# Kernel tuning notes

Hardware: AMD Instinct MI355X
Metric: run time of the kernel (lower is better)

The kernel has to match this reference:

```python
import jax, jax.numpy as jnp
import numpy as np

B, M, IN, H, D = 64, 512, 256, 4, 64
N = B * M
E = N * 16


def setup_inputs() -> dict:
    key = jax.random.key(0)
    ks = jax.random.split(key, 12)
    s = 1.0 / np.sqrt(IN)
    return {
        "query_input": jax.random.normal(ks[0], (N, IN), jnp.float32),
        "source_input": jax.random.normal(ks[1], (N, IN), jnp.float32),
        "edge_weight": jax.random.uniform(ks[2], (E,), jnp.float32),
        "Wq_w": jax.random.normal(ks[3], (IN, H * D), jnp.float32) * s,
        "Wq_b": jax.random.normal(ks[4], (H * D,), jnp.float32) * s,
        "Wk_w": jax.random.normal(ks[5], (IN, H * D), jnp.float32) * s,
        "Wk_b": jax.random.normal(ks[6], (H * D,), jnp.float32) * s,
        "Wv_w": jax.random.normal(ks[7], (IN, H * D), jnp.float32) * s,
        "Wv_b": jax.random.normal(ks[8], (H * D,), jnp.float32) * s,
        "n_nodes": jnp.full((B,), M, jnp.int32),
        "edge_index": jax.random.randint(ks[9], (2, E), 0, N, jnp.int32),
    }


def reference(query_input, source_input, edge_weight, Wq_w, Wq_b, Wk_w, Wk_b, Wv_w, Wv_b, n_nodes, edge_index):
    # projections -> [N, H, D]
    q = (query_input @ Wq_w + Wq_b).reshape(N, H, D)
    k = (source_input @ Wk_w + Wk_b).reshape(N, H, D)
    v = (source_input @ Wv_w + Wv_b).reshape(N, H, D)

    # 'simple' kernel attention. Global L2 normalization (torch.norm over whole tensor).
    qn = q / jnp.linalg.norm(q)
    kn = k / jnp.linalg.norm(k)
    # equal-size graphs: padding + mask reduces exactly to a reshape [B, M, H, D]
    q_pad = qn.reshape(B, M, H, D)
    k_pad = kn.reshape(B, M, H, D)
    v_pad = v.reshape(B, M, H, D)
    kv = jnp.einsum('bmhk,bmhv->bhkv', k_pad, v_pad)          # per-graph K^T V
    v_sum = v_pad.sum(axis=1)                                  # [B, H, D] scatter_add over batch
    k_sum = k_pad.sum(axis=1)                                  # [B, H, D]
    numer = jnp.einsum('bmhk,bhkv->bmhv', q_pad, kv) + v_sum[:, None]
    denom = jnp.einsum('bmhk,bhk->bmh', q_pad, k_sum) + n_nodes.astype(q.dtype)[:, None, None]
    attn = (numer / denom[..., None]).reshape(N, H, D)

    # gcn_conv on value: out[c] = sum_{e: col_e = c} w_e * rsqrt(deg[col_e]*deg[row_e]) * v[row_e]
    row, col = edge_index[0], edge_index[1]
    deg = jax.ops.segment_sum(jnp.ones((E,), jnp.float32), col, num_segments=N)
    val = edge_weight / jnp.sqrt(deg[col] * deg[row])
    val = jnp.nan_to_num(val, nan=0.0, posinf=0.0, neginf=0.0)
    gcn = jax.ops.segment_sum(val[:, None, None] * v[row], col, num_segments=N)

    return (attn + gcn).mean(axis=1)  # mean over heads -> [N, D]
```

## Files before the change

### kernel.cpp

```cpp
#include <hip/hip_runtime.h>
#include <hip/hip_bf16.h>

#define NN 32768
#define BB 64
#define MM 512
#define HH 4
#define DD 64
#define INF 256
#define HD 256
#define EE 524288
#define XSZ 8388608

typedef unsigned short ushort;
typedef unsigned int uint;
typedef short s16x8 __attribute__((ext_vector_type(8)));
typedef ushort u16x8 __attribute__((ext_vector_type(8)));
typedef float f32x4 __attribute__((ext_vector_type(4)));

__device__ __forceinline__ ushort f2bf(float f) {
    uint u = __float_as_uint(f);
    return (ushort)((u + 0x7fffu + ((u >> 16) & 1u)) >> 16);
}
__device__ __forceinline__ float bf2f(ushort u) {
    return __uint_as_float((uint)u << 16);
}
__device__ __forceinline__ uint pkbf(float x, float y) {
    __hip_bfloat162 h = __float22bfloat162_rn(make_float2(x, y));
    return *(uint*)&h;
}

#define GLD16(gp, lp) __builtin_amdgcn_global_load_lds( \
    (const __attribute__((address_space(1))) void*)(gp), \
    (__attribute__((address_space(3))) void*)(lp), 16, 0, 0)

__global__ __launch_bounds__(256) void prep_kernel(
    const float* __restrict__ Wq, const float* __restrict__ Wk,
    const float* __restrict__ Wv, ushort* __restrict__ WT,
    const int* __restrict__ ei, int* __restrict__ deg,
    const float* __restrict__ Xq, const float* __restrict__ Xs,
    ushort* __restrict__ xq16, ushort* __restrict__ xs16)
{
    const int bid = blockIdx.x;
    if (bid < 768) {
        const int id = bid * 256 + threadIdx.x;
        const int mat = id >> 16, rem = id & 65535;
        const int n = rem >> 8, kk = rem & 255;
        const float* W = (mat == 0) ? Wq : (mat == 1) ? Wk : Wv;
        WT[id] = f2bf(W[kk * 256 + n]);
    } else if (bid < 2816) {
        const int e = (bid - 768) * 256 + threadIdx.x;
        atomicAdd(&deg[ei[EE + e]], 1);
    } else {
        const size_t id = (size_t)(bid - 2816) * 256 + threadIdx.x;
        const size_t o8 = id * 8;
        const float* src; ushort* dst; size_t o;
        if (o8 < XSZ) { src = Xq; dst = xq16; o = o8; }
        else          { src = Xs; dst = xs16; o = o8 - XSZ; }
        const float4 f0 = *(const float4*)(src + o);
        const float4 f1 = *(const float4*)(src + o + 4);
        u16x8 r;
        r[0] = f2bf(f0.x); r[1] = f2bf(f0.y); r[2] = f2bf(f0.z); r[3] = f2bf(f0.w);
        r[4] = f2bf(f1.x); r[5] = f2bf(f1.y); r[6] = f2bf(f1.z); r[7] = f2bf(f1.w);
        *(u16x8*)(dst + o) = r;
    }
}

__global__ __launch_bounds__(256) void qkv_scan(
    const ushort* __restrict__ Xq16, const ushort* __restrict__ Xs16,
    const ushort* __restrict__ WT,
    const float* __restrict__ bq, const float* __restrict__ bk,
    const float* __restrict__ bv,
    ushort* __restrict__ qo, ushort* __restrict__ ko, ushort* __restrict__ vo,
    float* __restrict__ sumsq,
    const int* __restrict__ deg, int* __restrict__ offsets)
{
    __shared__ ushort As[3][128 * 32];
    __shared__ ushort Bs[3][128 * 32];
    __shared__ float wred[4];
    __shared__ int part[256];

    const int id = blockIdx.x;
    const int t = threadIdx.x;

    if (id == 1536) {
        const int base = t * 128;
        int s = 0;
        for (int i = 0; i < 128; ++i) s += deg[base + i];
        part[t] = s;
        __syncthreads();
        for (int off = 1; off < 256; off <<= 1) {
            int a = part[t];
            int b2 = (t >= off) ? part[t - off] : 0;
            __syncthreads();
            part[t] = a + b2;
            __syncthreads();
        }
        int run = (t == 0) ? 0 : part[t - 1];
        for (int i = 0; i < 128; ++i) { offsets[base + i] = run; run += deg[base + i]; }
        if (t == 255) offsets[NN] = run;
        return;
    }

    const int vv = (id & 7) * 192 + (id >> 3);
    const int rt = vv / 6, ct = vv % 6;
    const int wsel = ct >> 1;
    const ushort* A16 = (wsel == 0) ? Xq16 : Xs16;
    const ushort* W   = WT + (size_t)wsel * 65536;
    const float* bias = (wsel == 0) ? bq : (wsel == 1) ? bk : bv;
    ushort* C         = (wsel == 0) ? qo : (wsel == 1) ? ko : vo;
    const int row0 = rt * 128;
    const int col0 = (ct & 1) * 128;

    const int l = t & 63, w = t >> 6;
    const int fr = l & 15, q4 = l >> 4;
    const int wr = (w & 1) * 64, wc = (w >> 1) * 64;

    const int srow = (w << 4) + (l >> 2);
    const int scol = (l & 3) << 3;
    const ushort* ga = &A16[(size_t)(row0 + srow) * INF + scol];
    const ushort* gb = &W  [(size_t)(col0 + srow) * INF + scol];
    const int lbase = (w << 9);

    f32x4 acc[4][4] = {};

#define QKV_STAGE(bufi, k0) \
    GLD16(ga + (k0),            &As[bufi][lbase]); \
    GLD16(ga + (k0) + 64 * INF, &As[bufi][2048 + lbase]); \
    GLD16(gb + (k0),            &Bs[bufi][lbase]); \
    GLD16(gb + (k0) + 64 * INF, &Bs[bufi][2048 + lbase]);

#define QKV_COMPUTE(bufi) { \
    const int kg = q4 * 8; \
    s16x8 af[4], bfr[4]; \
    _Pragma("unroll") \
    for (int i = 0; i < 4; ++i) \
        af[i] = *(const s16x8*)&As[bufi][(wr + i * 16 + fr) * 32 + kg]; \
    _Pragma("unroll") \
    for (int j = 0; j < 4; ++j) \
        bfr[j] = *(const s16x8*)&Bs[bufi][(wc + j * 16 + fr) * 32 + kg]; \
    _Pragma("unroll") \
    for (int i = 0; i < 4; ++i) \
    _Pragma("unroll") \
        for (int j = 0; j < 4; ++j) \
            acc[i][j] = __builtin_amdgcn_mfma_f32_16x16x32_bf16( \
                af[i], bfr[j], acc[i][j], 0, 0, 0); }

#define WAIT4 asm volatile("s_waitcnt vmcnt(4)" ::: "memory")
#define WAIT0 asm volatile("s_waitcnt vmcnt(0)" ::: "memory")
#define BAR   __builtin_amdgcn_s_barrier()

    QKV_STAGE(0, 0)
    QKV_STAGE(1, 32)

    WAIT4; BAR; QKV_STAGE(2,  64) QKV_COMPUTE(0)
    WAIT4; BAR; QKV_STAGE(0,  96) QKV_COMPUTE(1)
    WAIT4; BAR; QKV_STAGE(1, 128) QKV_COMPUTE(2)
    WAIT4; BAR; QKV_STAGE(2, 160) QKV_COMPUTE(0)
    WAIT4; BAR; QKV_STAGE(0, 192) QKV_COMPUTE(1)
    WAIT4; BAR; QKV_STAGE(1, 224) QKV_COMPUTE(2)
    WAIT4; BAR;                   QKV_COMPUTE(0)
    WAIT0; BAR;                   QKV_COMPUTE(1)

    float loc = 0.f;
#pragma unroll
    for (int j = 0; j < 4; ++j) {
        const int colg = col0 + wc + j * 16 + fr;
        const float bj = bias[colg];
#pragma unroll
        for (int i = 0; i < 4; ++i) {
            const int rowg = row0 + wr + i * 16 + q4 * 4;
#pragma unroll
            for (int m = 0; m < 4; ++m) {
                float cv = acc[i][j][m] + bj;
                loc += cv * cv;
                C[(size_t)(rowg + m) * HD + colg] = f2bf(cv);
            }
        }
    }
    if (wsel < 2) {
#pragma unroll
        for (int off = 32; off > 0; off >>= 1) loc += __shfl_down(loc, off, 64);
        if (l == 0) wred[w] = loc;
        __syncthreads();
        if (t == 0) atomicAdd(&sumsq[wsel], wred[0] + wred[1] + wred[2] + wred[3]);
    }
}

#define KVP 72
__global__ __launch_bounds__(256) void kv_vbar_bucket(
    const ushort* __restrict__ k16, const ushort* __restrict__ v16,
    ushort* __restrict__ kv16, float* __restrict__ ksum_f, float* __restrict__ vsum_f,
    float* __restrict__ vbar,
    const int* __restrict__ ei, const float* __restrict__ ew,
    const int* __restrict__ deg, const int* __restrict__ offsets,
    int* __restrict__ cursor, int2* __restrict__ pairbuf)
{
    __shared__ ushort kT[64 * KVP];
    __shared__ ushort vT[64 * KVP];
    const int bid = blockIdx.x;
    const int t = threadIdx.x;

    if (bid >= 1280) {
        const int e = (bid - 1280) * 256 + t;
        const int row = ei[e], col = ei[EE + e];
        const long long prod = (long long)deg[row] * (long long)deg[col];
        float val = 0.f;
        if (prod > 0) val = ew[e] * __frsqrt_rn((float)prod);
        const int pos = atomicAdd(&cursor[col], 1);
        pairbuf[offsets[col] + pos] = make_int2(row, __float_as_int(val));
        return;
    }
    if (bid >= 256) {
        const int idx = (bid - 256) * 256 + t;
        const int n = idx >> 3, d0 = (idx & 7) * 8;
        const ushort* vr = &v16[(size_t)n * HD + d0];
        u16x8 v0 = *(const u16x8*)(vr);
        u16x8 v1 = *(const u16x8*)(vr + 64);
        u16x8 v2 = *(const u16x8*)(vr + 128);
        u16x8 v3 = *(const u16x8*)(vr + 192);
        float o[8];
#pragma unroll
        for (int j = 0; j < 8; ++j)
            o[j] = 0.25f * (bf2f(v0[j]) + bf2f(v1[j]) + bf2f(v2[j]) + bf2f(v3[j]));
        float* vb = &vbar[(size_t)n * DD + d0];
        *(float4*)(vb)     = make_float4(o[0], o[1], o[2], o[3]);
        *(float4*)(vb + 4) = make_float4(o[4], o[5], o[6], o[7]);
        return;
    }

    const int h = bid & 3, b = bid >> 2;
    const int l = t & 63, w = t >> 6;
    const size_t base = (size_t)b * MM * HD + (size_t)h * DD;

    const int fr = l & 15, q4 = l >> 4, kg = q4 * 8;
    const int wr2 = (w & 1) * 32, wc2 = (w >> 1) * 32;
    s16x8 ones;
#pragma unroll
    for (int i = 0; i < 8; ++i) ones[i] = (short)0x3F80;

    f32x4 acc[2][2] = {};
    f32x4 aks[2] = {};
    f32x4 avs[2] = {};

    const int mat = t >> 7;
    const int rem = t & 127;
    const int dq  = rem >> 5;
    const int u   = rem & 31;
    const int r0  = 2 * u;
    const int d0  = dq * 16;
    const ushort* src = mat ? v16 : k16;
    ushort* dst = mat ? vT : kT;

    for (int chunk = 0; chunk < 8; ++chunk) {
        const int m0 = chunk * 64;
        {
            const ushort* p0 = &src[base + (size_t)(m0 + r0) * HD + d0];
            const ushort* p1 = p0 + HD;
            u16x8 ra0 = *(const u16x8*)(p0);
            u16x8 ra1 = *(const u16x8*)(p0 + 8);
            u16x8 rb0 = *(const u16x8*)(p1);
            u16x8 rb1 = *(const u16x8*)(p1 + 8);
#pragma unroll
            for (int jj = 0; jj < 8; ++jj) {
                uint pk = (uint)ra0[jj] | ((uint)rb0[jj] << 16);
                *(uint*)&dst[(d0 + jj) * KVP + r0] = pk;
            }
#pragma unroll
            for (int jj = 0; jj < 8; ++jj) {
                uint pk = (uint)ra1[jj] | ((uint)rb1[jj] << 16);
                *(uint*)&dst[(d0 + 8 + jj) * KVP + r0] = pk;
            }
        }
        __syncthreads();

#pragma unroll
        for (int s = 0; s < 2; ++s) {
            const int mo = s * 32 + kg;
            s16x8 af[2], bf[2];
            af[0] = *(const s16x8*)&kT[(wr2 + fr) * KVP + mo];
            af[1] = *(const s16x8*)&kT[(wr2 + 16 + fr) * KVP + mo];
            bf[0] = *(const s16x8*)&vT[(wc2 + fr) * KVP + mo];
            bf[1] = *(const s16x8*)&vT[(wc2 + 16 + fr) * KVP + mo];
#pragma unroll
            for (int il = 0; il < 2; ++il)
#pragma unroll
                for (int jl = 0; jl < 2; ++jl)
                    acc[il][jl] = __builtin_amdgcn_mfma_f32_16x16x32_bf16(
                        af[il], bf[jl], acc[il][jl], 0, 0, 0);
#pragma unroll
            for (int il = 0; il < 2; ++il)
                aks[il] = __builtin_amdgcn_mfma_f32_16x16x32_bf16(
                    af[il], ones, aks[il], 0, 0, 0);
#pragma unroll
            for (int jl = 0; jl < 2; ++jl)
                avs[jl] = __builtin_amdgcn_mfma_f32_16x16x32_bf16(
                    ones, bf[jl], avs[jl], 0, 0, 0);
        }
        __syncthreads();
    }

    ushort* kvb = &kv16[((size_t)b * HH + h) * 4096];
#pragma unroll
    for (int jl = 0; jl < 2; ++jl) {
        const int dv = wc2 + 16 * jl + fr;
#pragma unroll
        for (int il = 0; il < 2; ++il) {
            const int dk = wr2 + 16 * il + q4 * 4;
            uint2 pk = make_uint2(pkbf(acc[il][jl][0], acc[il][jl][1]),
                                  pkbf(acc[il][jl][2], acc[il][jl][3]));
            *(uint2*)&kvb[(size_t)dv * 64 + dk] = pk;
        }
    }
    float* ksb = &ksum_f[((size_t)b * HH + h) * 64];
    float* vsb = &vsum_f[((size_t)b * HH + h) * 64];
    if (wc2 == 0 && fr == 0) {
#pragma unroll
        for (int il = 0; il < 2; ++il)
#pragma unroll
            for (int m = 0; m < 4; ++m)
                ksb[wr2 + 16 * il + q4 * 4 + m] = aks[il][m];
    }
    if (wr2 == 0 && l < 16) {
        vsb[wc2 + l]      = avs[0][0];
        vsb[wc2 + 16 + l] = avs[1][0];
    }
}

#define AKP 72
__global__ __launch_bounds__(256) void attn_mfma(
    const ushort* __restrict__ q16, const ushort* __restrict__ kv16,
    const float* __restrict__ ksum_f, const float* __restrict__ vsum_f,
    const float* __restrict__ sumsq,
    const int* __restrict__ n_nodes, float* __restrict__ out)
{
    const int b = blockIdx.y;
    const int m0 = blockIdx.x * 64;
    const int t = threadIdx.x;
    const int l = t & 63, w = t >> 6;
    const int fr = l & 15, q4 = l >> 4;
    const int wn = (w & 1) * 32, wd = (w >> 1) * 32;

    __shared__ ushort kvbf[HH][64 * AKP];
    __shared__ float ksum_l[HH][64], vsum_l[HH][64], denom_l[HH][64];

    const float nn = (float)n_nodes[b];
    const float inv = 1.0f / (sqrtf(sumsq[0]) * sqrtf(sumsq[1]));

    {
        const int dv = t >> 2, dk0 = (t & 3) * 16;
#pragma unroll
        for (int h = 0; h < HH; ++h) {
            const ushort* kvg = &kv16[((size_t)(b * HH + h)) * 4096 + dv * 64 + dk0];
            *(uint4*)&kvbf[h][dv * AKP + dk0]     = *(const uint4*)kvg;
            *(uint4*)&kvbf[h][dv * AKP + dk0 + 8] = *(const uint4*)(kvg + 8);
        }
        const int hh = t >> 6, dd = t & 63;
        ksum_l[hh][dd] = ksum_f[((size_t)(b * HH + hh)) * 64 + dd];
        vsum_l[hh][dd] = vsum_f[((size_t)(b * HH + hh)) * 64 + dd];
    }
    __syncthreads();

    {
        const int r = t & 63, hh = t >> 6;
        const ushort* qr = &q16[((size_t)(b * MM + m0 + r)) * HD + hh * DD];
        float dsum = 0.f;
#pragma unroll
        for (int c = 0; c < 8; ++c) {
            u16x8 qv = *(const u16x8*)(qr + 8 * c);
#pragma unroll
            for (int j2 = 0; j2 < 8; ++j2)
                dsum += bf2f(qv[j2]) * ksum_l[hh][8 * c + j2];
        }
        denom_l[hh][r] = nn + inv * dsum;
    }
    __syncthreads();

    f32x4 acco[2][2] = {};
#pragma unroll
    for (int h = 0; h < HH; ++h) {
        f32x4 pacc[2][2] = {};
#pragma unroll
        for (int kx = 0; kx < 2; ++kx) {
            const int k0 = kx * 32;
            s16x8 af[2], bfr[2];
#pragma unroll
            for (int il = 0; il < 2; ++il)
                af[il] = *(const s16x8*)&q16[
                    ((size_t)(b * MM + m0 + wn + 16 * il + fr)) * HD + h * DD + k0 + q4 * 8];
#pragma unroll
            for (int jl = 0; jl < 2; ++jl)
                bfr[jl] = *(const s16x8*)&kvbf[h][(wd + 16 * jl + fr) * AKP + k0 + q4 * 8];
#pragma unroll
            for (int il = 0; il < 2; ++il)
#pragma unroll
                for (int jl = 0; jl < 2; ++jl)
                    pacc[il][jl] = __builtin_amdgcn_mfma_f32_16x16x32_bf16(
                        af[il], bfr[jl], pacc[il][jl], 0, 0, 0);
        }
#pragma unroll
        for (int il = 0; il < 2; ++il)
#pragma unroll
            for (int m = 0; m < 4; ++m) {
                const float rden = 0.25f / denom_l[h][wn + 16 * il + q4 * 4 + m];
#pragma unroll
                for (int jl = 0; jl < 2; ++jl) {
                    const int d = wd + 16 * jl + fr;
                    acco[il][jl][m] += (inv * pacc[il][jl][m] + vsum_l[h][d]) * rden;
                }
            }
    }

#pragma unroll
    for (int il = 0; il < 2; ++il)
#pragma unroll
        for (int m = 0; m < 4; ++m) {
            const size_t node = (size_t)b * MM + m0 + wn + 16 * il + q4 * 4 + m;
#pragma unroll
            for (int jl = 0; jl < 2; ++jl)
                out[node * DD + wd + 16 * jl + fr] = acco[il][jl][m];
        }
}

__global__ __launch_bounds__(256) void gcn_gather(
    const int* __restrict__ offsets, const int2* __restrict__ pairbuf,
    const float* __restrict__ vbar, float* __restrict__ out)
{
    const int t = blockIdx.x * 256 + threadIdx.x;
    const int n = t >> 5;
    const int g = t & 31;
    const int d4 = (g & 15) << 2;
    const int grp = g >> 4;
    const int s = offsets[n], e = offsets[n + 1];
    float ax = 0.f, ay = 0.f, az = 0.f, aw = 0.f;
    int i = s + grp;
    for (; i + 2 < e; i += 4) {
        const int2 p0 = pairbuf[i], p1 = pairbuf[i + 2];
        const float w0 = __int_as_float(p0.y), w1 = __int_as_float(p1.y);
        const float4 v0 = *(const float4*)&vbar[(size_t)p0.x * DD + d4];
        const float4 v1 = *(const float4*)&vbar[(size_t)p1.x * DD + d4];
        ax += w0 * v0.x + w1 * v1.x;
        ay += w0 * v0.y + w1 * v1.y;
        az += w0 * v0.z + w1 * v1.z;
        aw += w0 * v0.w + w1 * v1.w;
    }
    if (i < e) {
        const int2 p = pairbuf[i];
        const float wv = __int_as_float(p.y);
        const float4 v = *(const float4*)&vbar[(size_t)p.x * DD + d4];
        ax += wv * v.x; ay += wv * v.y; az += wv * v.z; aw += wv * v.w;
    }
    ax += __shfl_xor(ax, 16, 64);
    ay += __shfl_xor(ay, 16, 64);
    az += __shfl_xor(az, 16, 64);
    aw += __shfl_xor(aw, 16, 64);
    if (grp == 0) {
        float4 o = *(float4*)&out[(size_t)n * DD + d4];
        o.x += ax; o.y += ay; o.z += az; o.w += aw;
        *(float4*)&out[(size_t)n * DD + d4] = o;
    }
}

extern "C" void kernel_launch(void* const* d_in, const int* in_sizes, int n_in,
                              void* d_out, int out_size, void* d_ws, size_t ws_size,
                              hipStream_t stream)
{
    (void)in_sizes; (void)n_in; (void)out_size; (void)ws_size;
    const float* Xq = (const float*)d_in[0];
    const float* Xs = (const float*)d_in[1];
    const float* ew = (const float*)d_in[2];
    const float* Wq = (const float*)d_in[3];
    const float* bq = (const float*)d_in[4];
    const float* Wk = (const float*)d_in[5];
    const float* bk = (const float*)d_in[6];
    const float* Wv = (const float*)d_in[7];
    const float* bv = (const float*)d_in[8];
    const int* n_nodes = (const int*)d_in[9];
    const int* ei = (const int*)d_in[10];
    float* out = (float*)d_out;
    float* ws  = (float*)d_ws;

    const size_t SZ_QKV   = (size_t)NN * HD / 2;
    const size_t OFF_Q    = 0;
    const size_t OFF_K    = SZ_QKV;
    const size_t OFF_V    = SZ_QKV * 2;
    const size_t OFF_SS   = SZ_QKV * 3;
    const size_t OFF_DEG  = OFF_SS + 16;
    const size_t OFF_CUR  = OFF_DEG + NN;
    const size_t OFF_WT   = OFF_CUR + NN;
    const size_t OFF_OFFS = OFF_WT + 3 * 65536 / 2;
    const size_t OFF_UNI  = OFF_OFFS + NN + 16;
    const size_t OFF_XQ16 = OFF_UNI;
    const size_t OFF_XS16 = OFF_UNI + XSZ / 2;
    const size_t OFF_KV16 = OFF_UNI;
    const size_t OFF_KSF  = OFF_KV16 + (size_t)BB * HH * 4096 / 2;
    const size_t OFF_VSF  = OFF_KSF + (size_t)BB * HH * 64;
    const size_t OFF_PAIR = OFF_VSF + (size_t)BB * HH * 64;
    const size_t OFF_VBAR = OFF_PAIR + 2 * (size_t)EE;

    ushort* q16   = (ushort*)(ws + OFF_Q);
    ushort* k16   = (ushort*)(ws + OFF_K);
    ushort* v16   = (ushort*)(ws + OFF_V);
    float* sumsq  = ws + OFF_SS;
    int*   deg    = (int*)(ws + OFF_DEG);
    int*   cursor = (int*)(ws + OFF_CUR);
    ushort* WT    = (ushort*)(ws + OFF_WT);
    int*   offs   = (int*)(ws + OFF_OFFS);
    ushort* xq16  = (ushort*)(ws + OFF_XQ16);
    ushort* xs16  = (ushort*)(ws + OFF_XS16);
    ushort* kv16  = (ushort*)(ws + OFF_KV16);
    float* ksum_f = ws + OFF_KSF;
    float* vsum_f = ws + OFF_VSF;
    int2*  pairb  = (int2*)(ws + OFF_PAIR);
    float* vbar   = ws + OFF_VBAR;

    hipMemsetAsync(sumsq, 0, (16 + 2 * NN) * sizeof(float), stream);
    prep_kernel<<<11008, 256, 0, stream>>>(Wq, Wk, Wv, WT, ei, deg, Xq, Xs, xq16, xs16);
    qkv_scan<<<1537, 256, 0, stream>>>(
        xq16, xs16, WT, bq, bk, bv, q16, k16, v16, sumsq, deg, offs);
    kv_vbar_bucket<<<3328, 256, 0, stream>>>(
        k16, v16, kv16, ksum_f, vsum_f, vbar, ei, ew, deg, offs, cursor, pairb);
    attn_mfma<<<dim3(MM / 64, BB), 256, 0, stream>>>(
        q16, kv16, ksum_f, vsum_f, sumsq, n_nodes, out);
    gcn_gather<<<(NN * 32) / 256, 256, 0, stream>>>(offs, pairb, vbar, out);
}
```

Before: 248.0 us.

## Fuse fp32-to-bf16 input conversion into QKV GEMM A-tile loading

Removes the separate pass in prep_kernel that converted query and source inputs to bf16 buffers. The QKV GEMM now loads fp32 A tiles into registers, packs them to bf16 and writes them to LDS, while B tiles still use direct global-to-LDS loads, which changes the pipeline to register-staged A with double buffering. This avoids writing and re-reading the bf16 copies of the inputs, at the cost of more register pressure and VALU conversion work inside the GEMM, and A rows are now re-read in fp32 by each column tile. The epilogue also packs bf16 pairs with a hardware conversion.

New measurement: 243.9 us. No clear change (-1.7%).

```diff
diff --git a/kernel.cpp b/kernel.cpp
--- a/kernel.cpp
+++ b/kernel.cpp
@@ -9,7 +9,6 @@
 #define INF 256
 #define HD 256
 #define EE 524288
-#define XSZ 8388608
 
 typedef unsigned short ushort;
 typedef unsigned int uint;
@@ -36,9 +35,7 @@
 __global__ __launch_bounds__(256) void prep_kernel(
     const float* __restrict__ Wq, const float* __restrict__ Wk,
     const float* __restrict__ Wv, ushort* __restrict__ WT,
-    const int* __restrict__ ei, int* __restrict__ deg,
-    const float* __restrict__ Xq, const float* __restrict__ Xs,
-    ushort* __restrict__ xq16, ushort* __restrict__ xs16)
+    const int* __restrict__ ei, int* __restrict__ deg)
 {
     const int bid = blockIdx.x;
     if (bid < 768) {
@@ -47,26 +44,14 @@
         const int n = rem >> 8, kk = rem & 255;
         const float* W = (mat == 0) ? Wq : (mat == 1) ? Wk : Wv;
         WT[id] = f2bf(W[kk * 256 + n]);
-    } else if (bid < 2816) {
+    } else {
         const int e = (bid - 768) * 256 + threadIdx.x;
         atomicAdd(&deg[ei[EE + e]], 1);
-    } else {
-        const size_t id = (size_t)(bid - 2816) * 256 + threadIdx.x;
-        const size_t o8 = id * 8;
-        const float* src; ushort* dst; size_t o;
-        if (o8 < XSZ) { src = Xq; dst = xq16; o = o8; }
-        else          { src = Xs; dst = xs16; o = o8 - XSZ; }
-        const float4 f0 = *(const float4*)(src + o);
-        const float4 f1 = *(const float4*)(src + o + 4);
-        u16x8 r;
-        r[0] = f2bf(f0.x); r[1] = f2bf(f0.y); r[2] = f2bf(f0.z); r[3] = f2bf(f0.w);
-        r[4] = f2bf(f1.x); r[5] = f2bf(f1.y); r[6] = f2bf(f1.z); r[7] = f2bf(f1.w);
-        *(u16x8*)(dst + o) = r;
     }
 }
 
 __global__ __launch_bounds__(256) void qkv_scan(
-    const ushort* __restrict__ Xq16, const ushort* __restrict__ Xs16,
+    const float* __restrict__ Xq, const float* __restrict__ Xs,
     const ushort* __restrict__ WT,
     const float* __restrict__ bq, const float* __restrict__ bk,
     const float* __restrict__ bv,
@@ -74,7 +59,7 @@
     float* __restrict__ sumsq,
     const int* __restrict__ deg, int* __restrict__ offsets)
 {
-    __shared__ ushort As[3][128 * 32];
+    __shared__ ushort As[2][128 * 32];
     __shared__ ushort Bs[3][128 * 32];
     __shared__ float wred[4];
     __shared__ int part[256];
@@ -104,7 +89,7 @@
     const int vv = (id & 7) * 192 + (id >> 3);
     const int rt = vv / 6, ct = vv % 6;
     const int wsel = ct >> 1;
-    const ushort* A16 = (wsel == 0) ? Xq16 : Xs16;
+    const float* A    = (wsel == 0) ? Xq : Xs;
     const ushort* W   = WT + (size_t)wsel * 65536;
     const float* bias = (wsel == 0) ? bq : (wsel == 1) ? bk : bv;
     ushort* C         = (wsel == 0) ? qo : (wsel == 1) ? ko : vo;
@@ -117,27 +102,41 @@
 
     const int srow = (w << 4) + (l >> 2);
     const int scol = (l & 3) << 3;
-    const ushort* ga = &A16[(size_t)(row0 + srow) * INF + scol];
-    const ushort* gb = &W  [(size_t)(col0 + srow) * INF + scol];
+    const float*  ga = &A[(size_t)(row0 + srow) * INF + scol];
+    const ushort* gb = &W[(size_t)(col0 + srow) * INF + scol];
     const int lbase = (w << 9);
 
     f32x4 acc[4][4] = {};
-
-#define QKV_STAGE(bufi, k0) \
-    GLD16(ga + (k0),            &As[bufi][lbase]); \
-    GLD16(ga + (k0) + 64 * INF, &As[bufi][2048 + lbase]); \
-    GLD16(gb + (k0),            &Bs[bufi][lbase]); \
-    GLD16(gb + (k0) + 64 * INF, &Bs[bufi][2048 + lbase]);
-
-#define QKV_COMPUTE(bufi) { \
+    float4 a00, a01, a10, a11;
+
+#define QKV_ALOAD(k0) { \
+    const float* p0 = ga + (k0); \
+    const float* p1 = ga + (k0) + 64 * INF; \
+    a00 = *(const float4*)(p0);     a01 = *(const float4*)(p0 + 4); \
+    a10 = *(const float4*)(p1);     a11 = *(const float4*)(p1 + 4); }
+
+#define QKV_AWRITE(abuf) { \
+    union { u16x8 v; uint u[4]; } c0, c1; \
+    c0.u[0] = pkbf(a00.x, a00.y); c0.u[1] = pkbf(a00.z, a00.w); \
+    c0.u[2] = pkbf(a01.x, a01.y); c0.u[3] = pkbf(a01.z, a01.w); \
+    c1.u[0] = pkbf(a10.x, a10.y); c1.u[1] = pkbf(a10.z, a10.w); \
+    c1.u[2] = pkbf(a11.x, a11.y); c1.u[3] = pkbf(a11.z, a11.w); \
+    *(u16x8*)&As[abuf][srow * 32 + scol]        = c0.v; \
+    *(u16x8*)&As[abuf][2048 + srow * 32 + scol] = c1.v; }
+
+#define QKV_BSTAGE(bbuf, k0) \
+    GLD16(gb + (k0),            &Bs[bbuf][lbase]); \
+    GLD16(gb + (k0) + 64 * INF, &Bs[bbuf][2048 + lbase]);
+
+#define QKV_COMPUTE(abuf, bbuf) { \
     const int kg = q4 * 8; \
     s16x8 af[4], bfr[4]; \
     _Pragma("unroll") \
     for (int i = 0; i < 4; ++i) \
-        af[i] = *(const s16x8*)&As[bufi][(wr + i * 16 + fr) * 32 + kg]; \
+        af[i] = *(const s16x8*)&As[abuf][(wr + i * 16 + fr) * 32 + kg]; \
     _Pragma("unroll") \
     for (int j = 0; j < 4; ++j) \
-        bfr[j] = *(const s16x8*)&Bs[bufi][(wc + j * 16 + fr) * 32 + kg]; \
+        bfr[j] = *(const s16x8*)&Bs[bbuf][(wc + j * 16 + fr) * 32 + kg]; \
     _Pragma("unroll") \
     for (int i = 0; i < 4; ++i) \
     _Pragma("unroll") \
@@ -145,21 +144,30 @@
             acc[i][j] = __builtin_amdgcn_mfma_f32_16x16x32_bf16( \
                 af[i], bfr[j], acc[i][j], 0, 0, 0); }
 
-#define WAIT4 asm volatile("s_waitcnt vmcnt(4)" ::: "memory")
-#define WAIT0 asm volatile("s_waitcnt vmcnt(0)" ::: "memory")
-#define BAR   __builtin_amdgcn_s_barrier()
-
-    QKV_STAGE(0, 0)
-    QKV_STAGE(1, 32)
-
-    WAIT4; BAR; QKV_STAGE(2,  64) QKV_COMPUTE(0)
-    WAIT4; BAR; QKV_STAGE(0,  96) QKV_COMPUTE(1)
-    WAIT4; BAR; QKV_STAGE(1, 128) QKV_COMPUTE(2)
-    WAIT4; BAR; QKV_STAGE(2, 160) QKV_COMPUTE(0)
-    WAIT4; BAR; QKV_STAGE(0, 192) QKV_COMPUTE(1)
-    WAIT4; BAR; QKV_STAGE(1, 224) QKV_COMPUTE(2)
-    WAIT4; BAR;                   QKV_COMPUTE(0)
-    WAIT0; BAR;                   QKV_COMPUTE(1)
+#define WAITN(n) asm volatile("s_waitcnt vmcnt(" #n ")" ::: "memory")
+#define LGKM0   asm volatile("s_waitcnt lgkmcnt(0)" ::: "memory")
+#define BAR     __builtin_amdgcn_s_barrier()
+
+    QKV_ALOAD(0)
+    QKV_BSTAGE(0, 0)
+    QKV_BSTAGE(1, 32)
+
+    WAITN(4); QKV_AWRITE(0) LGKM0; BAR;
+    QKV_ALOAD(32)  QKV_BSTAGE(2, 64)   WAITN(8); QKV_COMPUTE(0, 0)
+    WAITN(2); QKV_AWRITE(1) LGKM0; BAR;
+    QKV_ALOAD(64)  QKV_BSTAGE(0, 96)   WAITN(8); QKV_COMPUTE(1, 1)
+    WAITN(2); QKV_AWRITE(0) LGKM0; BAR;
+    QKV_ALOAD(96)  QKV_BSTAGE(1, 128)  WAITN(8); QKV_COMPUTE(0, 2)
+    WAITN(2); QKV_AWRITE(1) LGKM0; BAR;
+    QKV_ALOAD(128) QKV_BSTAGE(2, 160)  WAITN(8); QKV_COMPUTE(1, 0)
+    WAITN(2); QKV_AWRITE(0) LGKM0; BAR;
+    QKV_ALOAD(160) QKV_BSTAGE(0, 192)  WAITN(8); QKV_COMPUTE(0, 1)
+    WAITN(2); QKV_AWRITE(1) LGKM0; BAR;
+    QKV_ALOAD(192) QKV_BSTAGE(1, 224)  WAITN(8); QKV_COMPUTE(1, 2)
+    WAITN(2); QKV_AWRITE(0) LGKM0; BAR;
+    QKV_ALOAD(224)                     WAITN(6); QKV_COMPUTE(0, 0)
+    WAITN(0); QKV_AWRITE(1) LGKM0; BAR;
+    QKV_COMPUTE(1, 1)
 
     float loc = 0.f;
 #pragma unroll
@@ -169,12 +177,17 @@
 #pragma unroll
         for (int i = 0; i < 4; ++i) {
             const int rowg = row0 + wr + i * 16 + q4 * 4;
-#pragma unroll
-            for (int m = 0; m < 4; ++m) {
-                float cv = acc[i][j][m] + bj;
-                loc += cv * cv;
-                C[(size_t)(rowg + m) * HD + colg] = f2bf(cv);
-            }
+            const float cv0 = acc[i][j][0] + bj;
+            const float cv1 = acc[i][j][1] + bj;
+            const float cv2 = acc[i][j][2] + bj;
+            const float cv3 = acc[i][j][3] + bj;
+            loc += cv0 * cv0 + cv1 * cv1 + cv2 * cv2 + cv3 * cv3;
+            const uint p01 = pkbf(cv0, cv1);
+            const uint p23 = pkbf(cv2, cv3);
+            C[(size_t)(rowg + 0) * HD + colg] = (ushort)p01;
+            C[(size_t)(rowg + 1) * HD + colg] = (ushort)(p01 >> 16);
+            C[(size_t)(rowg + 2) * HD + colg] = (ushort)p23;
+            C[(size_t)(rowg + 3) * HD + colg] = (ushort)(p23 >> 16);
         }
     }
     if (wsel < 2) {
@@ -488,10 +501,7 @@
     const size_t OFF_CUR  = OFF_DEG + NN;
     const size_t OFF_WT   = OFF_CUR + NN;
     const size_t OFF_OFFS = OFF_WT + 3 * 65536 / 2;
-    const size_t OFF_UNI  = OFF_OFFS + NN + 16;
-    const size_t OFF_XQ16 = OFF_UNI;
-    const size_t OFF_XS16 = OFF_UNI + XSZ / 2;
-    const size_t OFF_KV16 = OFF_UNI;
+    const size_t OFF_KV16 = OFF_OFFS + NN + 16;
     const size_t OFF_KSF  = OFF_KV16 + (size_t)BB * HH * 4096 / 2;
     const size_t OFF_VSF  = OFF_KSF + (size_t)BB * HH * 64;
     const size_t OFF_PAIR = OFF_VSF + (size_t)BB * HH * 64;
@@ -505,8 +515,6 @@
     int*   cursor = (int*)(ws + OFF_CUR);
     ushort* WT    = (ushort*)(ws + OFF_WT);
     int*   offs   = (int*)(ws + OFF_OFFS);
-    ushort* xq16  = (ushort*)(ws + OFF_XQ16);
-    ushort* xs16  = (ushort*)(ws + OFF_XS16);
     ushort* kv16  = (ushort*)(ws + OFF_KV16);
     float* ksum_f = ws + OFF_KSF;
     float* vsum_f = ws + OFF_VSF;
@@ -514,9 +522,9 @@
     float* vbar   = ws + OFF_VBAR;
 
     hipMemsetAsync(sumsq, 0, (16 + 2 * NN) * sizeof(float), stream);
-    prep_kernel<<<11008, 256, 0, stream>>>(Wq, Wk, Wv, WT, ei, deg, Xq, Xs, xq16, xs16);
+    prep_kernel<<<2816, 256, 0, stream>>>(Wq, Wk, Wv, WT, ei, deg);
     qkv_scan<<<1537, 256, 0, stream>>>(
-        xq16, xs16, WT, bq, bk, bv, q16, k16, v16, sumsq, deg, offs);
+        Xq, Xs, WT, bq, bk, bv, q16, k16, v16, sumsq, deg, offs);
     kv_vbar_bucket<<<3328, 256, 0, stream>>>(
         k16, v16, kv16, ksum_f, vsum_f, vbar, ei, ew, deg, offs, cursor, pairb);
     attn_mfma<<<dim3(MM / 64, BB), 256, 0, stream>>>(
```
